# Performance work log

Measured on AMD Instinct MI355X. Metric: run time of the kernel, lower is better.

Reference implementation:

```python
import jax, jax.numpy as jnp
import numpy as np

K = 16          # k_neighbors
C = 1.0         # Poincare ball curvature
ALPHA = 0.1     # residual blend strength
EPS = 1e-5


def poincare_project(x, c=C):
    # clip points to lie strictly inside the ball of radius 1/sqrt(c)
    norm = jnp.linalg.norm(x, axis=-1, keepdims=True)
    max_norm = (1.0 - EPS) / jnp.sqrt(c)
    scale = jnp.where(norm > max_norm, max_norm / jnp.maximum(norm, EPS), 1.0)
    return x * scale


def poincare_cdist(x, y, c=C):
    # x: [Nq, d], y: [M, d] -> [Nq, M] pairwise Poincare-ball distances
    x2 = jnp.sum(x * x, axis=-1)                       # [Nq]
    y2 = jnp.sum(y * y, axis=-1)                       # [M]
    xy = x @ y.T                                       # [Nq, M]
    sq = jnp.maximum(x2[:, None] + y2[None, :] - 2.0 * xy, 0.0)
    denom = (1.0 - c * x2)[:, None] * (1.0 - c * y2)[None, :]
    arg = 1.0 + 2.0 * c * sq / jnp.maximum(denom, EPS)
    return jnp.arccosh(jnp.maximum(arg, 1.0 + EPS)) / jnp.sqrt(c)


def layernorm(x, g, b):
    mu = jnp.mean(x, axis=-1, keepdims=True)
    var = jnp.var(x, axis=-1, keepdims=True)
    return (x - mu) * jax.lax.rsqrt(var + EPS) * g + b


def setup_inputs() -> dict:
    key = jax.random.key(0)
    ks = jax.random.split(key, 6)
    Nq, H, D, M = 2048, 1024, 256, 65536
    s1 = 1.0 / np.sqrt(H)
    s2 = 1.0 / np.sqrt(D)
    return {
        "hidden": jax.random.normal(ks[0], (Nq, H), jnp.float32),
        "memory": jax.random.normal(ks[1], (M, D), jnp.float32) * 0.1,
        "w1": jax.random.normal(ks[2], (H, D), jnp.float32) * s1,
        "b1": jnp.zeros((D,), jnp.float32),
        "ln_g": jnp.ones((D,), jnp.float32),
        "ln_b": jnp.zeros((D,), jnp.float32),
        "w2": jax.random.normal(ks[3], (D, D), jnp.float32) * s2,
        "b2": jnp.zeros((D,), jnp.float32),
        "wp": jax.random.normal(ks[4], (D, H), jnp.float32) * s2,
        "bp": jnp.zeros((H,), jnp.float32),
    }


def reference(hidden, memory, w1, b1, ln_g, ln_b, w2, b2, wp, bp):
    # query network: Linear -> LayerNorm -> GELU(exact) -> Linear
    q = layernorm(hidden @ w1 + b1, ln_g, ln_b)
    q = jax.nn.gelu(q, approximate=False) @ w2 + b2          # [Nq, D]

    # project query and memory bank onto the Poincare ball
    q_b = poincare_project(q)
    m_b = poincare_project(memory)

    # hyperbolic kNN: full pairwise distances, then top-k smallest
    dist = poincare_cdist(q_b, m_b)                          # [Nq, M]
    neg_topk, idx = jax.lax.top_k(-dist, K)                  # [Nq, K]

    # distance-weighted aggregation of retrieved memories
    w = jax.nn.softmax(neg_topk, axis=-1)                    # softmax(-dist)
    retrieved = jnp.einsum("nk,nkd->nd", w, m_b[idx])        # [Nq, D]

    # project back to hidden space, residual blend
    out = hidden + ALPHA * (retrieved @ wp + bp)             # [Nq, H]
    return out
```

## Files before the change

kernel.cpp:

```cpp
#include <hip/hip_runtime.h>
#include <hip/hip_bf16.h>

typedef unsigned int u32;
typedef unsigned short u16;
typedef unsigned char u8;
typedef __attribute__((ext_vector_type(8))) short short8;
typedef __attribute__((ext_vector_type(4))) float f32x4;
typedef __attribute__((ext_vector_type(4))) int i32x4;
typedef __attribute__((ext_vector_type(8))) int i32x8;

#define EPSV 1e-5f
#define MAXN (1.0f - 1e-5f)
#define THETA 0.17f
#define CAP 512
#define LCAPW 384u

__device__ __forceinline__ u16 f2bf(float f) {
    union { float f; u32 u; } v; v.f = f;
    u32 u = v.u;
    u32 r = (u + 0x7fffu + ((u >> 16) & 1u)) >> 16;
    return (u16)r;
}
__device__ __forceinline__ float bf2f(u16 h) {
    union { u32 u; float f; } v; v.u = ((u32)h) << 16;
    return v.f;
}
__device__ __forceinline__ u32 pk_fp8x4(float a, float b, float c, float d) {
    int v = __builtin_amdgcn_cvt_pk_fp8_f32(a, b, 0, false);
    v = __builtin_amdgcn_cvt_pk_fp8_f32(c, d, v, true);
    return (u32)v;
}
__device__ __forceinline__ u8 f2fp8(float a) {
    return (u8)(__builtin_amdgcn_cvt_pk_fp8_f32(a, a, 0, false) & 0xFF);
}

typedef __attribute__((address_space(1))) const unsigned char gbuf_t;
typedef __attribute__((address_space(3))) unsigned char lbuf_t;
__device__ __forceinline__ void gl2lds16(const void* g, void* l) {
    __builtin_amdgcn_global_load_lds((gbuf_t*)g, (lbuf_t*)l, 16, 0, 0);
}

__global__ __launch_bounds__(256) void k_pre(const float* __restrict__ mem,
                                             u8* __restrict__ mbf8,
                                             float* __restrict__ scale_m,
                                             float* __restrict__ y2m,
                                             u32* __restrict__ cnt,
                                             const float* __restrict__ hidden, u16* __restrict__ hb,
                                             const float* __restrict__ w1, u16* __restrict__ w1t,
                                             const float* __restrict__ w2, u16* __restrict__ w2t,
                                             const float* __restrict__ wp, u16* __restrict__ wpt) {
    __shared__ float ld[64 * 65];
    const int b = blockIdx.x, t = threadIdx.x;
    if (b < 16384) {
        int zi = b * 256 + t;
        if (zi < 2048) cnt[zi] = 0;
        const int row = b * 4 + (t >> 6);
        const int lane = t & 63;
        const float4* p = (const float4*)(mem + (size_t)row * 256);
        float4 v = p[lane];
        float ss = v.x * v.x + v.y * v.y + v.z * v.z + v.w * v.w;
#pragma unroll
        for (int off = 32; off; off >>= 1) ss += __shfl_xor(ss, off);
        float norm = sqrtf(ss);
        float scale = (norm > MAXN) ? MAXN / fmaxf(norm, EPSV) : 1.0f;
        float x0 = v.x * scale, x1 = v.y * scale, x2 = v.z * scale, x3 = v.w * scale;
        *(u32*)&mbf8[(size_t)row * 256 + lane * 4] = pk_fp8x4(x0, x1, x2, x3);
        if (lane == 0) { y2m[row] = ss * scale * scale; scale_m[row] = scale; }
    } else if (b < 18432) {
        int i = (b - 16384) * 256 + t;
        float4 v = ((const float4*)hidden)[i];
        ushort4 u; u.x = f2bf(v.x); u.y = f2bf(v.y); u.z = f2bf(v.z); u.w = f2bf(v.w);
        ((ushort4*)hb)[i] = u;
    } else {
        const float* src; u16* dst; int K, N, tile;
        int bb = b - 18432;
        if (bb < 64)      { src = w1; dst = w1t; K = 1024; N = 256;  tile = bb; }
        else if (bb < 80) { src = w2; dst = w2t; K = 256;  N = 256;  tile = bb - 64; }
        else              { src = wp; dst = wpt; K = 256;  N = 1024; tile = bb - 80; }
        int ntn = N >> 6;
        int tk = (tile / ntn) * 64, tn = (tile - (tile / ntn) * ntn) * 64;
#pragma unroll
        for (int j = 0; j < 16; ++j) {
            int lin = j * 256 + t;
            int r = lin >> 6, c = lin & 63;
            ld[r * 65 + c] = src[(size_t)(tk + r) * N + tn + c];
        }
        __syncthreads();
#pragma unroll
        for (int j = 0; j < 16; ++j) {
            int lin = j * 256 + t;
            int c2 = lin >> 6, r2 = lin & 63;
            dst[(size_t)(tn + c2) * K + tk + r2] = f2bf(ld[r2 * 65 + c2]);
        }
    }
}

__global__ __launch_bounds__(256) void k_qnet(const u16* __restrict__ hb,
                                              const u16* __restrict__ w1t,
                                              const float* __restrict__ b1,
                                              const float* __restrict__ lng,
                                              const float* __restrict__ lnb,
                                              const u16* __restrict__ w2t,
                                              const float* __restrict__ b2,
                                              u8* __restrict__ qb8,
                                              float* __restrict__ x2q) {
    __shared__ float sm[16 * 260];
    __shared__ u16 qs[16 * 264];
    const int t = threadIdx.x;
    const int w = t >> 6, lane = t & 63;
    const int l16 = lane & 15, kq = (lane >> 4) * 8, rbase = (lane >> 4) * 4;
    const int q0 = blockIdx.x * 16;
    f32x4 zero = {0.f, 0.f, 0.f, 0.f};

    {
        f32x4 acc[4] = {zero, zero, zero, zero};
        const u16* ap = hb + (size_t)(q0 + l16) * 1024 + kq;
        for (int k0 = 0; k0 < 1024; k0 += 32) {
            short8 av = *(const short8*)(ap + k0);
#pragma unroll
            for (int ct = 0; ct < 4; ++ct) {
                int n = w * 64 + ct * 16 + l16;
                short8 bv = *(const short8*)&w1t[(size_t)n * 1024 + k0 + kq];
                acc[ct] = __builtin_amdgcn_mfma_f32_16x16x32_bf16(av, bv, acc[ct], 0, 0, 0);
            }
        }
#pragma unroll
        for (int ct = 0; ct < 4; ++ct) {
            int n = w * 64 + ct * 16 + l16;
            float bias = b1[n];
#pragma unroll
            for (int r = 0; r < 4; ++r)
                sm[(rbase + r) * 260 + n] = acc[ct][r] + bias;
        }
    }
    __syncthreads();
    {
        const int row = t >> 4, sub = t & 15;
        float s1 = 0.f, s2 = 0.f;
#pragma unroll
        for (int i = 0; i < 16; ++i) {
            float v = sm[row * 260 + sub + 16 * i];
            s1 += v; s2 += v * v;
        }
#pragma unroll
        for (int off = 8; off; off >>= 1) {
            s1 += __shfl_xor(s1, off, 16);
            s2 += __shfl_xor(s2, off, 16);
        }
        float mu = s1 * (1.0f / 256.0f);
        float var = s2 * (1.0f / 256.0f) - mu * mu;
        float rstd = rsqrtf(var + EPSV);
#pragma unroll
        for (int i = 0; i < 16; ++i) {
            int cc = sub + 16 * i;
            float v = sm[row * 260 + cc];
            float xn = (v - mu) * rstd * lng[cc] + lnb[cc];
            float ge = 0.5f * xn * (1.0f + erff(xn * 0.7071067811865475f));
            qs[row * 264 + cc] = f2bf(ge);
        }
    }
    __syncthreads();
    f32x4 acc2[4] = {zero, zero, zero, zero};
    for (int k0 = 0; k0 < 256; k0 += 32) {
        short8 av = *(const short8*)&qs[l16 * 264 + k0 + kq];
#pragma unroll
        for (int ct = 0; ct < 4; ++ct) {
            int n = w * 64 + ct * 16 + l16;
            short8 bv = *(const short8*)&w2t[(size_t)n * 256 + k0 + kq];
            acc2[ct] = __builtin_amdgcn_mfma_f32_16x16x32_bf16(av, bv, acc2[ct], 0, 0, 0);
        }
    }
    __syncthreads();
#pragma unroll
    for (int ct = 0; ct < 4; ++ct) {
        int n = w * 64 + ct * 16 + l16;
        float bias = b2[n];
#pragma unroll
        for (int r = 0; r < 4; ++r)
            sm[(rbase + r) * 260 + n] = acc2[ct][r] + bias;
    }
    __syncthreads();
    {
        const int row = t >> 4, sub = t & 15;
        float s2 = 0.f;
#pragma unroll
        for (int i = 0; i < 16; ++i) {
            float v = sm[row * 260 + sub + 16 * i];
            s2 += v * v;
        }
#pragma unroll
        for (int off = 8; off; off >>= 1) s2 += __shfl_xor(s2, off, 16);
        float norm = sqrtf(s2);
        float scale = (norm > MAXN) ? MAXN / fmaxf(norm, EPSV) : 1.0f;
        if (sub == 0) x2q[q0 + row] = s2 * scale * scale;
#pragma unroll
        for (int i = 0; i < 16; ++i) {
            int cc = sub + 16 * i;
            qb8[(size_t)(q0 + row) * 256 + cc] = f2fp8(sm[row * 260 + cc] * scale);
        }
    }
}

__global__ __launch_bounds__(256, 2) void k_dist(const u8* __restrict__ qb8,
                                                 const u8* __restrict__ mbf8,
                                                 u32* __restrict__ cnt,
                                                 uint2* __restrict__ cand) {
    __shared__ __align__(16) u8 ring[65536];
    __shared__ uint2 candW[4 * LCAPW];
    __shared__ u32 wcntS[4];
    const int b = blockIdx.x;
    const int xcd = b & 7;
    const int idx = b >> 3;
    const int qt = idx >> 1;
    const int mg = xcd * 2 + (idx & 1);
    const int q0 = qt * 64;
    const int m0 = mg * 4096;
    const int t = threadIdx.x;
    const int w = t >> 6, lane = t & 63;
    const int l16 = lane & 15, Q = lane >> 4, rbase = Q * 4;

#pragma unroll
    for (int j = 0; j < 4; ++j) {
        int s = j * 256 + t;
        int r = s >> 4, p = s & 15;
        int c = p ^ (r & 15);
        gl2lds16(qb8 + (size_t)(q0 + r) * 256 + c * 16, ring + s * 16);
    }
    __syncthreads();

    i32x8 av[4][2];
#pragma unroll
    for (int i = 0; i < 4; ++i) {
        int R = i * 16 + l16;
        int aoff = R * 256 + (((Q * 2) ^ l16) << 4);
#pragma unroll
        for (int st = 0; st < 2; ++st) {
            i32x4 lo = *(const i32x4*)(ring + (aoff ^ (st << 7)));
            i32x4 hi = *(const i32x4*)(ring + (aoff ^ (st << 7) ^ 16));
            av[i][st] = __builtin_shufflevector(lo, hi, 0, 1, 2, 3, 4, 5, 6, 7);
        }
    }
    __syncthreads();

    const int rl = (lane >> 4);
    const int pch = lane & 15;
    const u8* pB[8];
#pragma unroll
    for (int i = 0; i < 8; ++i) {
        int rr = i * 4 + rl;
        int c = pch ^ (rr & 15);
        pB[i] = mbf8 + (size_t)(m0 + w * 32 + rr) * 256 + c * 16;
    }
    u8* const wring = ring + w * 16384;
    const int ldst = lane * 16;

#pragma unroll
    for (int i = 0; i < 8; ++i) gl2lds16(pB[i], wring + i * 1024 + ldst);
#pragma unroll
    for (int i = 0; i < 8; ++i) gl2lds16(pB[i] + 32768, wring + 8192 + i * 1024 + ldst);

    const int boff0 = l16 * 256 + (((Q * 2) ^ l16) << 4);
    const int boff1 = boff0 + 4096;

    f32x4 zero = {0.f, 0.f, 0.f, 0.f};
    u32 wcnt = 0;
    const u32 mgbase = (u32)(m0 + w * 32 + l16);

#pragma unroll 1
    for (int mt = 0; mt < 32; ++mt) {
        if (mt < 31) { asm volatile("s_waitcnt vmcnt(8)" ::: "memory"); }
        else         { asm volatile("s_waitcnt vmcnt(0)" ::: "memory"); }
        const u8* bufp = wring + ((mt & 1) << 13);
        i32x4 a00 = *(const i32x4*)(bufp + boff0);
        i32x4 a01 = *(const i32x4*)(bufp + (boff0 ^ 16));
        i32x4 a10 = *(const i32x4*)(bufp + (boff0 ^ 128));
        i32x4 a11 = *(const i32x4*)(bufp + (boff0 ^ 128 ^ 16));
        i32x4 c00 = *(const i32x4*)(bufp + boff1);
        i32x4 c01 = *(const i32x4*)(bufp + (boff1 ^ 16));
        i32x4 c10 = *(const i32x4*)(bufp + (boff1 ^ 128));
        i32x4 c11 = *(const i32x4*)(bufp + (boff1 ^ 128 ^ 16));
        asm volatile("s_waitcnt lgkmcnt(0)" ::: "memory");
        __builtin_amdgcn_sched_barrier(0);
        if (mt < 30) {
            const size_t so = (size_t)(mt + 2) * 32768;
            u8* d = (u8*)bufp;
#pragma unroll
            for (int i = 0; i < 8; ++i) gl2lds16(pB[i] + so, d + i * 1024 + ldst);
        }
        i32x8 bv00 = __builtin_shufflevector(a00, a01, 0, 1, 2, 3, 4, 5, 6, 7);
        i32x8 bv10 = __builtin_shufflevector(a10, a11, 0, 1, 2, 3, 4, 5, 6, 7);
        i32x8 bv01 = __builtin_shufflevector(c00, c01, 0, 1, 2, 3, 4, 5, 6, 7);
        i32x8 bv11 = __builtin_shufflevector(c10, c11, 0, 1, 2, 3, 4, 5, 6, 7);
        f32x4 acc[4][2];
#pragma unroll
        for (int i = 0; i < 4; ++i) { acc[i][0] = zero; acc[i][1] = zero; }
#pragma unroll
        for (int i = 0; i < 4; ++i) {
            acc[i][0] = __builtin_amdgcn_mfma_scale_f32_16x16x128_f8f6f4(
                av[i][0], bv00, acc[i][0], 0, 0, 0, 0x7F7F7F7F, 0, 0x7F7F7F7F);
            acc[i][1] = __builtin_amdgcn_mfma_scale_f32_16x16x128_f8f6f4(
                av[i][0], bv01, acc[i][1], 0, 0, 0, 0x7F7F7F7F, 0, 0x7F7F7F7F);
        }
#pragma unroll
        for (int i = 0; i < 4; ++i) {
            acc[i][0] = __builtin_amdgcn_mfma_scale_f32_16x16x128_f8f6f4(
                av[i][1], bv10, acc[i][0], 0, 0, 0, 0x7F7F7F7F, 0, 0x7F7F7F7F);
            acc[i][1] = __builtin_amdgcn_mfma_scale_f32_16x16x128_f8f6f4(
                av[i][1], bv11, acc[i][1], 0, 0, 0, 0x7F7F7F7F, 0, 0x7F7F7F7F);
        }
        const u32 mglob = mgbase + (u32)(mt * 128);
#pragma unroll
        for (int i = 0; i < 4; ++i)
#pragma unroll
            for (int cf = 0; cf < 2; ++cf)
#pragma unroll
                for (int r = 0; r < 4; ++r) {
                    float d = acc[i][cf][r];
                    unsigned long long mask = __ballot(d > THETA);
                    if (mask) {
                        if (d > THETA) {
                            u32 pos = wcnt + (u32)__popcll(mask & ((1ull << lane) - 1ull));
                            if (pos < LCAPW)
                                candW[w * LCAPW + pos] =
                                    make_uint2(((u32)(i * 16 + rbase + r) << 16) |
                                               (mglob + (u32)(cf * 16)),
                                               __float_as_uint(d));
                        }
                        wcnt += (u32)__popcll(mask);
                    }
                }
    }

    if (lane == 0) wcntS[w] = wcnt;
    __syncthreads();
#pragma unroll 1
    for (int wv = 0; wv < 4; ++wv) {
        u32 n = wcntS[wv]; if (n > LCAPW) n = LCAPW;
        for (u32 i = (u32)t; i < n; i += 256u) {
            uint2 e = candW[wv * LCAPW + i];
            int q = q0 + (int)(e.x >> 16);
            u32 pos = atomicAdd(&cnt[q], 1u);
            if (pos < CAP) cand[(size_t)q * CAP + pos] = make_uint2(e.x & 0xFFFFu, e.y);
        }
    }
}

__global__ __launch_bounds__(64, 4) void k_merge(const u32* __restrict__ cnt,
                                                 const uint2* __restrict__ cand,
                                                 const float* __restrict__ x2q,
                                                 const float* __restrict__ y2m,
                                                 const float* __restrict__ scale_m,
                                                 const float* __restrict__ mem,
                                                 u16* __restrict__ rb) {
    const int q = blockIdx.x;
    const int lane = threadIdx.x;
    int n = (int)cnt[q]; if (n > CAP) n = CAP;
    const float x2 = x2q[q];
    const float dx = 1.0f - x2;
    float rv[8]; u32 mi[8];
#pragma unroll
    for (int j = 0; j < 8; ++j) {
        int idx = lane + 64 * j;
        rv[j] = 3.0e38f; mi[j] = 0;
        if (idx < n) {
            uint2 c = cand[(size_t)q * CAP + idx];
            float dot = __uint_as_float(c.y);
            float y2 = y2m[c.x];
            float sq = fmaxf(x2 + y2 - 2.0f * dot, 0.0f);
            float den = fmaxf(dx * (1.0f - y2), EPSV);
            rv[j] = sq / den;
            mi[j] = c.x;
        }
    }
    __shared__ float sdist[16];
    __shared__ u32 smi[16];
    __shared__ float swt[16];
    for (int k = 0; k < 16; ++k) {
        float lm = rv[0]; int ls = 0;
#pragma unroll
        for (int j = 1; j < 8; ++j) if (rv[j] < lm) { lm = rv[j]; ls = j; }
        unsigned long long key = (((unsigned long long)__float_as_uint(lm)) << 32) | (u32)(lane * 8 + ls);
#pragma unroll
        for (int off = 32; off; off >>= 1) {
            unsigned long long o = __shfl_xor(key, off);
            key = (o < key) ? o : key;
        }
        u32 sid = (u32)(key & 0xffffffffu);
        int wl = (int)(sid >> 3), wslot = (int)(sid & 7);
        if (lane == wl) {
            sdist[k] = rv[wslot];
            smi[k] = mi[wslot];
            rv[wslot] = 3.0e38f;
        }
    }
    __syncthreads();
    float rr = sdist[lane & 15];
    float arg = fmaxf(fmaf(2.0f, rr, 1.0f), 1.0f + EPSV);
    float dneg = -acoshf(arg);
    float mx = dneg;
#pragma unroll
    for (int off = 8; off; off >>= 1) mx = fmaxf(mx, __shfl_xor(mx, off, 16));
    float e = expf(dneg - mx);
    float ssum = e;
#pragma unroll
    for (int off = 8; off; off >>= 1) ssum += __shfl_xor(ssum, off, 16);
    if (lane < 16) swt[lane] = e / ssum;
    __syncthreads();
    float acc[4] = {0.f, 0.f, 0.f, 0.f};
    for (int k = 0; k < 16; ++k) {
        u32 row = smi[k];
        float wks = swt[k] * scale_m[row];
        const float* mr = mem + (size_t)row * 256;
#pragma unroll
        for (int j = 0; j < 4; ++j) acc[j] += wks * mr[lane + 64 * j];
    }
#pragma unroll
    for (int j = 0; j < 4; ++j) rb[(size_t)q * 256 + lane + 64 * j] = f2bf(acc[j]);
}

__global__ __launch_bounds__(256) void k_out(const u16* __restrict__ rb,
                                             const u16* __restrict__ wpt,
                                             const float* __restrict__ bp,
                                             const float* __restrict__ hidden,
                                             float* __restrict__ out) {
    const int b = blockIdx.x;
    const int mt = b & 31, nt = b >> 5;
    const int t = threadIdx.x;
    const int w = t >> 6, lane = t & 63;
    const int l16 = lane & 15, kq = (lane >> 4) * 8, rbase = (lane >> 4) * 4;
    const int n = nt * 64 + w * 16 + l16;
    f32x4 zero = {0.f, 0.f, 0.f, 0.f};
    f32x4 acc[4] = {zero, zero, zero, zero};
    for (int k0 = 0; k0 < 256; k0 += 32) {
        short8 bv = *(const short8*)&wpt[(size_t)n * 256 + k0 + kq];
#pragma unroll
        for (int rt = 0; rt < 4; ++rt) {
            short8 av = *(const short8*)&rb[(size_t)(mt * 64 + rt * 16 + l16) * 256 + k0 + kq];
            acc[rt] = __builtin_amdgcn_mfma_f32_16x16x32_bf16(av, bv, acc[rt], 0, 0, 0);
        }
    }
    float bpn = bp[n];
#pragma unroll
    for (int rt = 0; rt < 4; ++rt)
#pragma unroll
        for (int r = 0; r < 4; ++r) {
            int m = mt * 64 + rt * 16 + rbase + r;
            out[(size_t)m * 1024 + n] = hidden[(size_t)m * 1024 + n] + 0.1f * (acc[rt][r] + bpn);
        }
}

extern "C" void kernel_launch(void* const* d_in, const int* in_sizes, int n_in,
                              void* d_out, int out_size, void* d_ws, size_t ws_size,
                              hipStream_t stream) {
    const float* hidden = (const float*)d_in[0];
    const float* memory = (const float*)d_in[1];
    const float* w1 = (const float*)d_in[2];
    const float* b1 = (const float*)d_in[3];
    const float* ln_g = (const float*)d_in[4];
    const float* ln_b = (const float*)d_in[5];
    const float* w2 = (const float*)d_in[6];
    const float* b2 = (const float*)d_in[7];
    const float* wp = (const float*)d_in[8];
    const float* bp = (const float*)d_in[9];
    float* out = (float*)d_out;
    char* ws = (char*)d_ws;

    float* scale_m = (float*)(ws);
    float* y2m = (float*)(ws + 33554432);
    u16* hb   = (u16*)(ws + 33816576);
    u16* w1t  = (u16*)(ws + 38010880);
    u16* w2t  = (u16*)(ws + 38535168);
    u16* wpt  = (u16*)(ws + 38666240);
    u8*  qb8  = (u8*)(ws + 40239104);
    float* x2q = (float*)(ws + 41287680);
    u32* cnt  = (u32*)(ws + 41295872);
    uint2* cand = (uint2*)(ws + 41304064);
    u16* rb   = (u16*)(ws + 49692672);
    u8*  mbf8 = (u8*)(ws + 50741248);

    hipLaunchKernelGGL(k_pre, dim3(18576), dim3(256), 0, stream,
                       memory, mbf8, scale_m, y2m, cnt, hidden, hb, w1, w1t, w2, w2t, wp, wpt);
    hipLaunchKernelGGL(k_qnet, dim3(128), dim3(256), 0, stream,
                       hb, w1t, b1, ln_g, ln_b, w2t, b2, qb8, x2q);
    hipLaunchKernelGGL(k_dist, dim3(512), dim3(256), 0, stream, qb8, mbf8, cnt, cand);
    hipLaunchKernelGGL(k_merge, dim3(2048), dim3(64), 0, stream, cnt, cand, x2q, y2m, scale_m, memory, rb);
    hipLaunchKernelGGL(k_out, dim3(512), dim3(256), 0, stream, rb, wpt, bp, hidden, out);
}
```

Measured before the change: 261.0 us.

## Fuse query network into memory preprocessing kernel and convert hidden to bf16 inline

Splits the weight transpose into its own small kernel and merges the query-network GEMM/LayerNorm blocks with the memory-bank projection blocks in one launch, so the 128 qnet blocks run concurrently with the memory-prep work instead of serially. The separate hidden-to-bf16 conversion pass and its workspace buffer are removed; the qnet loads fp32 hidden and converts to bf16 in registers. This trades an extra launch for weight transposes and more global read bytes for hidden per qnet block against removing a serialized low-occupancy kernel.

```diff
diff --git a/kernel.cpp b/kernel.cpp
--- a/kernel.cpp
+++ b/kernel.cpp
@@ -40,21 +40,55 @@
     __builtin_amdgcn_global_load_lds((gbuf_t*)g, (lbuf_t*)l, 16, 0, 0);
 }
 
-__global__ __launch_bounds__(256) void k_pre(const float* __restrict__ mem,
-                                             u8* __restrict__ mbf8,
-                                             float* __restrict__ scale_m,
-                                             float* __restrict__ y2m,
-                                             u32* __restrict__ cnt,
-                                             const float* __restrict__ hidden, u16* __restrict__ hb,
-                                             const float* __restrict__ w1, u16* __restrict__ w1t,
-                                             const float* __restrict__ w2, u16* __restrict__ w2t,
-                                             const float* __restrict__ wp, u16* __restrict__ wpt) {
+__global__ __launch_bounds__(256) void k_w(const float* __restrict__ w1, u16* __restrict__ w1t,
+                                           const float* __restrict__ w2, u16* __restrict__ w2t,
+                                           const float* __restrict__ wp, u16* __restrict__ wpt) {
     __shared__ float ld[64 * 65];
+    const int bb = blockIdx.x, t = threadIdx.x;
+    const float* src; u16* dst; int K, N, tile;
+    if (bb < 64)      { src = w1; dst = w1t; K = 1024; N = 256;  tile = bb; }
+    else if (bb < 80) { src = w2; dst = w2t; K = 256;  N = 256;  tile = bb - 64; }
+    else              { src = wp; dst = wpt; K = 256;  N = 1024; tile = bb - 80; }
+    int ntn = N >> 6;
+    int tk = (tile / ntn) * 64, tn = (tile - (tile / ntn) * ntn) * 64;
+#pragma unroll
+    for (int j = 0; j < 16; ++j) {
+        int lin = j * 256 + t;
+        int r = lin >> 6, c = lin & 63;
+        ld[r * 65 + c] = src[(size_t)(tk + r) * N + tn + c];
+    }
+    __syncthreads();
+#pragma unroll
+    for (int j = 0; j < 16; ++j) {
+        int lin = j * 256 + t;
+        int c2 = lin >> 6, r2 = lin & 63;
+        dst[(size_t)(tn + c2) * K + tk + r2] = f2bf(ld[r2 * 65 + c2]);
+    }
+}
+
+__global__ __launch_bounds__(256) void k_fused(const float* __restrict__ mem,
+                                               u8* __restrict__ mbf8,
+                                               float* __restrict__ scale_m,
+                                               float* __restrict__ y2m,
+                                               u32* __restrict__ cnt,
+                                               const float* __restrict__ hidden,
+                                               const u16* __restrict__ w1t,
+                                               const float* __restrict__ b1,
+                                               const float* __restrict__ lng,
+                                               const float* __restrict__ lnb,
+                                               const u16* __restrict__ w2t,
+                                               const float* __restrict__ b2,
+                                               u8* __restrict__ qb8,
+                                               float* __restrict__ x2q) {
+    __shared__ float sm[16 * 260];
+    __shared__ u16 qs[16 * 264];
     const int b = blockIdx.x, t = threadIdx.x;
-    if (b < 16384) {
-        int zi = b * 256 + t;
+
+    if (b >= 128) {
+        const int bb = b - 128;
+        int zi = bb * 256 + t;
         if (zi < 2048) cnt[zi] = 0;
-        const int row = b * 4 + (t >> 6);
+        const int row = bb * 4 + (t >> 6);
         const int lane = t & 63;
         const float4* p = (const float4*)(mem + (size_t)row * 256);
         float4 v = p[lane];
@@ -66,57 +100,25 @@
         float x0 = v.x * scale, x1 = v.y * scale, x2 = v.z * scale, x3 = v.w * scale;
         *(u32*)&mbf8[(size_t)row * 256 + lane * 4] = pk_fp8x4(x0, x1, x2, x3);
         if (lane == 0) { y2m[row] = ss * scale * scale; scale_m[row] = scale; }
-    } else if (b < 18432) {
-        int i = (b - 16384) * 256 + t;
-        float4 v = ((const float4*)hidden)[i];
-        ushort4 u; u.x = f2bf(v.x); u.y = f2bf(v.y); u.z = f2bf(v.z); u.w = f2bf(v.w);
-        ((ushort4*)hb)[i] = u;
-    } else {
-        const float* src; u16* dst; int K, N, tile;
-        int bb = b - 18432;
-        if (bb < 64)      { src = w1; dst = w1t; K = 1024; N = 256;  tile = bb; }
-        else if (bb < 80) { src = w2; dst = w2t; K = 256;  N = 256;  tile = bb - 64; }
-        else              { src = wp; dst = wpt; K = 256;  N = 1024; tile = bb - 80; }
-        int ntn = N >> 6;
-        int tk = (tile / ntn) * 64, tn = (tile - (tile / ntn) * ntn) * 64;
-#pragma unroll
-        for (int j = 0; j < 16; ++j) {
-            int lin = j * 256 + t;
-            int r = lin >> 6, c = lin & 63;
-            ld[r * 65 + c] = src[(size_t)(tk + r) * N + tn + c];
-        }
-        __syncthreads();
-#pragma unroll
-        for (int j = 0; j < 16; ++j) {
-            int lin = j * 256 + t;
-            int c2 = lin >> 6, r2 = lin & 63;
-            dst[(size_t)(tn + c2) * K + tk + r2] = f2bf(ld[r2 * 65 + c2]);
-        }
-    }
-}
-
-__global__ __launch_bounds__(256) void k_qnet(const u16* __restrict__ hb,
-                                              const u16* __restrict__ w1t,
-                                              const float* __restrict__ b1,
-                                              const float* __restrict__ lng,
-                                              const float* __restrict__ lnb,
-                                              const u16* __restrict__ w2t,
-                                              const float* __restrict__ b2,
-                                              u8* __restrict__ qb8,
-                                              float* __restrict__ x2q) {
-    __shared__ float sm[16 * 260];
-    __shared__ u16 qs[16 * 264];
-    const int t = threadIdx.x;
+        return;
+    }
+
     const int w = t >> 6, lane = t & 63;
     const int l16 = lane & 15, kq = (lane >> 4) * 8, rbase = (lane >> 4) * 4;
-    const int q0 = blockIdx.x * 16;
+    const int q0 = b * 16;
     f32x4 zero = {0.f, 0.f, 0.f, 0.f};
 
     {
         f32x4 acc[4] = {zero, zero, zero, zero};
-        const u16* ap = hb + (size_t)(q0 + l16) * 1024 + kq;
+        const float* apf = hidden + (size_t)(q0 + l16) * 1024 + kq;
         for (int k0 = 0; k0 < 1024; k0 += 32) {
-            short8 av = *(const short8*)(ap + k0);
+            float4 f0 = *(const float4*)(apf + k0);
+            float4 f1 = *(const float4*)(apf + k0 + 4);
+            short8 av;
+            av[0] = (short)f2bf(f0.x); av[1] = (short)f2bf(f0.y);
+            av[2] = (short)f2bf(f0.z); av[3] = (short)f2bf(f0.w);
+            av[4] = (short)f2bf(f1.x); av[5] = (short)f2bf(f1.y);
+            av[6] = (short)f2bf(f1.z); av[7] = (short)f2bf(f1.w);
 #pragma unroll
             for (int ct = 0; ct < 4; ++ct) {
                 int n = w * 64 + ct * 16 + l16;
@@ -467,7 +469,6 @@
 
     float* scale_m = (float*)(ws);
     float* y2m = (float*)(ws + 33554432);
-    u16* hb   = (u16*)(ws + 33816576);
     u16* w1t  = (u16*)(ws + 38010880);
     u16* w2t  = (u16*)(ws + 38535168);
     u16* wpt  = (u16*)(ws + 38666240);
@@ -478,10 +479,11 @@
     u16* rb   = (u16*)(ws + 49692672);
     u8*  mbf8 = (u8*)(ws + 50741248);
 
-    hipLaunchKernelGGL(k_pre, dim3(18576), dim3(256), 0, stream,
-                       memory, mbf8, scale_m, y2m, cnt, hidden, hb, w1, w1t, w2, w2t, wp, wpt);
-    hipLaunchKernelGGL(k_qnet, dim3(128), dim3(256), 0, stream,
-                       hb, w1t, b1, ln_g, ln_b, w2t, b2, qb8, x2q);
+    hipLaunchKernelGGL(k_w, dim3(144), dim3(256), 0, stream,
+                       w1, w1t, w2, w2t, wp, wpt);
+    hipLaunchKernelGGL(k_fused, dim3(16512), dim3(256), 0, stream,
+                       memory, mbf8, scale_m, y2m, cnt, hidden,
+                       w1t, b1, ln_g, ln_b, w2t, b2, qb8, x2q);
     hipLaunchKernelGGL(k_dist, dim3(512), dim3(256), 0, stream, qb8, mbf8, cnt, cand);
     hipLaunchKernelGGL(k_merge, dim3(2048), dim3(64), 0, stream, cnt, cand, x2q, y2m, scale_m, memory, rb);
     hipLaunchKernelGGL(k_out, dim3(512), dim3(256), 0, stream, rb, wpt, bp, hidden, out);
```

Measured after the change: 274.1 us. +5.0%, slower.
